# Kernel tuning notes

Measured on AMD Instinct MI355X. Metric: run time of the kernel, lower is better.

The kernel has to match this reference:

```python
import jax, jax.numpy as jnp
import numpy as np

EPS = 1e-12


def _phi(e):
    # e: [C, L] -> pairwise euclidean distances [C, C], diagonal zeroed
    sq = jnp.sum(e * e, axis=1)                      # [C]
    prod = e @ e.T                                   # [C, C]
    d2 = sq[:, None] + sq[None, :] - 2.0 * prod
    d = jnp.sqrt(jnp.clip(d2, EPS, None))
    C = e.shape[0]
    return d * (1.0 - jnp.eye(C, dtype=e.dtype))


def setup_inputs() -> dict:
    key = jax.random.key(0)
    k1, k2, k3 = jax.random.split(key, 3)
    N, C, L = 64, 512, 256
    le_student = jax.random.normal(k1, (N, C, L), dtype=jnp.float32)
    le_teacher = jax.random.normal(k2, (N, C, L), dtype=jnp.float32)
    targets = jax.random.randint(k3, (N, C), 0, 2, dtype=jnp.int32)
    return {"le_student": le_student, "le_teacher": le_teacher, "targets": targets}


def reference(le_student, le_teacher, targets):
    N, C, L = le_student.shape
    m = targets.astype(le_student.dtype)             # [N, C] 0/1 mask
    es = le_student * m[:, :, None]                  # zero out negative rows
    et = le_teacher * m[:, :, None]

    Ds = jax.vmap(_phi)(es)                          # [N, C, C]
    Dt = jax.vmap(_phi)(et)                          # [N, C, C]

    eye = jnp.eye(C, dtype=m.dtype)
    pm = m[:, :, None] * m[:, None, :]               # pairs of positive rows
    offdiag = pm * (1.0 - eye)                       # off-diagonal positive pairs

    npos = jnp.sum(m, axis=1)                        # [N]
    cnt = npos * (npos - 1.0)                        # entries with d > 0 in submatrix
    valid = npos > 1.0
    safe_cnt = jnp.maximum(cnt, 1.0)

    mean_s = jnp.sum(Ds * offdiag, axis=(1, 2)) / safe_cnt
    mean_t = jax.lax.stop_gradient(jnp.sum(Dt * offdiag, axis=(1, 2)) / safe_cnt)
    mean_s = jnp.where(valid, mean_s, 1.0)
    mean_t = jnp.where(valid, mean_t, 1.0)

    d = Ds / mean_s[:, None, None]
    td = jax.lax.stop_gradient(Dt / mean_t[:, None, None])

    diff = d - td
    adiff = jnp.abs(diff)
    huber = jnp.where(adiff < 1.0, 0.5 * diff * diff, adiff - 0.5)

    per = jnp.sum(huber * pm, axis=(1, 2)) / jnp.maximum(npos, 1.0)
    return jnp.sum(jnp.where(valid, per, 0.0))
```

## Files before the change

### kernel.cpp

```cpp
#include <hip/hip_runtime.h>
#include <hip/hip_bf16.h>
#include <hip/hip_fp16.h>
#include <math.h>

#define NB 64
#define CC 512
#define LL 256

typedef __attribute__((ext_vector_type(4))) float floatx4;
typedef __attribute__((ext_vector_type(8))) short short8;

static __device__ __forceinline__ unsigned f2bf2(float x, float y) {
    __hip_bfloat162 h = __float22bfloat162_rn(make_float2(x, y));
    union { __hip_bfloat162 h; unsigned u; } c; c.h = h;
    return c.u;
}
static __device__ __forceinline__ unsigned short f2h(float x) {
    __half h = __float2half_rn(x);
    union { __half h; unsigned short u; } c; c.h = h;
    return c.u;
}
static __device__ __forceinline__ float h2f(unsigned u) {
    union { unsigned short u; __half h; } c; c.u = (unsigned short)u;
    return __half2float(c.h);
}

__global__ __launch_bounds__(256) void prep_kernel(
    const int* __restrict__ targets,
    int* __restrict__ idx, int* __restrict__ npos,
    float* __restrict__ sumS, float* __restrict__ sumT, float* __restrict__ out)
{
    const int n = blockIdx.x, tid = threadIdx.x;
    __shared__ int s_cnt[8], s_off[8];
    const int w = tid >> 6, lane = tid & 63;
    const int* tg = targets + n * CC;
    const bool p0 = tg[tid] != 0;
    const bool p1 = tg[tid + 256] != 0;
    const unsigned long long m0 = __ballot(p0);
    const unsigned long long m1 = __ballot(p1);
    if (lane == 0) { s_cnt[w] = __popcll(m0); s_cnt[4 + w] = __popcll(m1); }
    __syncthreads();
    if (tid == 0) {
        int a = 0;
        for (int i = 0; i < 8; ++i) { s_off[i] = a; a += s_cnt[i]; }
        npos[n] = a;
        sumS[n] = 0.0f; sumT[n] = 0.0f;
        if (n == 0) out[0] = 0.0f;
    }
    __syncthreads();
    const unsigned long long below = (1ull << lane) - 1ull;
    if (p0) idx[n * CC + s_off[w] + __popcll(m0 & below)] = tid;
    if (p1) idx[n * CC + s_off[4 + w] + __popcll(m1 & below)] = tid + 256;
}

static __device__ __forceinline__ bool decode_tile(int t, int u, int& tI, int& tJ) {
    if (t >= (u * (u + 1)) >> 1) return false;
    tI = 0;
    while (t >= u - tI) { t -= u - tI; ++tI; }
    tJ = tI + t;
    return true;
}

__global__ __launch_bounds__(256) void dist_kernel(
    const float* __restrict__ S, const float* __restrict__ T,
    const int* __restrict__ idx, const int* __restrict__ npos,
    float* __restrict__ sumS, float* __restrict__ sumT,
    unsigned short* __restrict__ Ds, unsigned short* __restrict__ Dt)
{
    const int bx = blockIdx.x;
    const int n = bx & (NB - 1);
    const int q = bx >> 6;
    const int mat = q & 1, t = q >> 1;
    const int np = npos[n];
    if (np < 2) return;
    int tI, tJ;
    if (!decode_tile(t, (np + 63) >> 6, tI, tJ)) return;
    const bool diag = (tI == tJ);

    __shared__ __align__(16) unsigned short lds[2][2][64][40];
    __shared__ float s_norm[2][64];
    __shared__ float red[4];

    const int tid = threadIdx.x;
    const int w = tid >> 6, lane = tid & 63;

    const float* P = (mat ? T : S) + (size_t)n * CC * LL;
    unsigned short* Dout = (mat ? Dt : Ds) + (((size_t)t * NB + n) << 12);
    float* sumP = mat ? sumT : sumS;

    const int srow = w * 32 + (lane >> 1);
    const int half = lane & 1;
    const bool stager = diag ? (srow < 64) : true;
    const int ab = srow >> 6, rloc = srow & 63;
    const int gk = (ab ? tJ : tI) * 64 + rloc;
    const int row = idx[n * CC + ((gk < np) ? gk : 0)];
    const char* rp = (const char*)P + (size_t)row * (LL * 4) + half * 64;

    float4 pre[4];
    float nsum = 0.0f;
    if (stager) {
        #pragma unroll
        for (int i = 0; i < 4; ++i) pre[i] = *(const float4*)(rp + i * 16);
    }

    const int m16 = lane & 15, quad = lane >> 4;
    const int bufB = diag ? 0 : 1;
    const int wrow = w * 16;

    floatx4 acc[4];
    #pragma unroll
    for (int c = 0; c < 4; ++c) { acc[c][0] = 0; acc[c][1] = 0; acc[c][2] = 0; acc[c][3] = 0; }

    for (int kk = 0; kk < 8; ++kk) {
        const int pb = kk & 1;
        if (stager) {
            #pragma unroll
            for (int i = 0; i < 4; ++i)
                nsum += pre[i].x * pre[i].x + pre[i].y * pre[i].y +
                        pre[i].z * pre[i].z + pre[i].w * pre[i].w;
            unsigned short* dst = &lds[ab][pb][rloc][half * 16];
            *(uint2*)(dst + 0)  = make_uint2(f2bf2(pre[0].x, pre[0].y), f2bf2(pre[0].z, pre[0].w));
            *(uint2*)(dst + 4)  = make_uint2(f2bf2(pre[1].x, pre[1].y), f2bf2(pre[1].z, pre[1].w));
            *(uint2*)(dst + 8)  = make_uint2(f2bf2(pre[2].x, pre[2].y), f2bf2(pre[2].z, pre[2].w));
            *(uint2*)(dst + 12) = make_uint2(f2bf2(pre[3].x, pre[3].y), f2bf2(pre[3].z, pre[3].w));
        }
        __syncthreads();
        if (stager && kk < 7) {
            #pragma unroll
            for (int i = 0; i < 4; ++i)
                pre[i] = *(const float4*)(rp + (kk + 1) * 128 + i * 16);
        }
        const short8 a = *(const short8*)&lds[0][pb][wrow + m16][quad * 8];
        #pragma unroll
        for (int c = 0; c < 4; ++c) {
            const short8 b = *(const short8*)&lds[bufB][pb][c * 16 + m16][quad * 8];
            acc[c] = __builtin_amdgcn_mfma_f32_16x16x32_bf16(a, b, acc[c], 0, 0, 0);
        }
    }

    if (stager) {
        const float v = nsum + __shfl_xor(nsum, 1);
        if (half == 0) s_norm[ab][rloc] = v;
    }
    __syncthreads();

    float l0 = 0.0f;
    #pragma unroll
    for (int c = 0; c < 4; ++c) {
        const int colL = c * 16 + m16;
        const int gj = tJ * 64 + colL;
        const float nB = s_norm[bufB][colL];
        #pragma unroll
        for (int r = 0; r < 4; ++r) {
            const int rowL = wrow + quad * 4 + r;
            const int gi = tI * 64 + rowL;
            const float d = sqrtf(fmaxf(s_norm[0][rowL] + nB - 2.0f * acc[c][r], 1e-12f));
            if (gi < np && gj < np && gi != gj) l0 += d;
            Dout[rowL * 64 + colL] = f2h(d);
        }
    }

    #pragma unroll
    for (int o = 32; o; o >>= 1) l0 += __shfl_down(l0, o);
    if (lane == 0) red[w] = l0;
    __syncthreads();
    if (tid == 0) {
        const float wgt = diag ? 1.0f : 2.0f;
        atomicAdd(sumP + n, wgt * (red[0] + red[1] + red[2] + red[3]));
    }
}

__global__ __launch_bounds__(256) void huber_kernel(
    const unsigned short* __restrict__ Ds, const unsigned short* __restrict__ Dt,
    const int* __restrict__ npos,
    const float* __restrict__ sumS, const float* __restrict__ sumT,
    float* __restrict__ out)
{
    const int bx = blockIdx.x;
    const int n = bx & (NB - 1), t = bx >> 6;
    const int np = npos[n];
    if (np < 2) return;
    int tI, tJ;
    if (!decode_tile(t, (np + 63) >> 6, tI, tJ)) return;

    const float cnt = (float)np * (float)(np - 1);
    const float inv_ms = cnt / sumS[n];
    const float inv_mt = cnt / sumT[n];

    const size_t slot = ((size_t)t * NB + n) << 12;
    const uint4* ps = (const uint4*)(Ds + slot);
    const uint4* pt = (const uint4*)(Dt + slot);
    const int tid = threadIdx.x;

    float h = 0.0f;
    #pragma unroll
    for (int it = 0; it < 2; ++it) {
        const int g = it * 256 + tid;
        const uint4 a = ps[g];
        const uint4 b = pt[g];
        const unsigned aw[4] = { a.x, a.y, a.z, a.w };
        const unsigned bw[4] = { b.x, b.y, b.z, b.w };
        const int e0 = g * 8;
        #pragma unroll
        for (int k = 0; k < 8; ++k) {
            const int e = e0 + k;
            const int gi = tI * 64 + (e >> 6);
            const int gj = tJ * 64 + (e & 63);
            if (gi < np && gj < np && gi != gj) {
                const unsigned wa = aw[k >> 1], wb = bw[k >> 1];
                const float ds = h2f((k & 1) ? (wa >> 16) : (wa & 0xffffu));
                const float dt = h2f((k & 1) ? (wb >> 16) : (wb & 0xffffu));
                const float diff = ds * inv_ms - dt * inv_mt;
                const float ad = fabsf(diff);
                h += (ad < 1.0f) ? 0.5f * diff * diff : ad - 0.5f;
            }
        }
    }

    #pragma unroll
    for (int o = 32; o; o >>= 1) h += __shfl_down(h, o);
    __shared__ float red[4];
    const int w = tid >> 6, lane = tid & 63;
    if (lane == 0) red[w] = h;
    __syncthreads();
    if (tid == 0) {
        const float wgt = (tI == tJ) ? 1.0f : 2.0f;
        atomicAdd(out, wgt * (red[0] + red[1] + red[2] + red[3]) / (float)np);
    }
}

extern "C" void kernel_launch(void* const* d_in, const int* in_sizes, int n_in,
                              void* d_out, int out_size, void* d_ws, size_t ws_size,
                              hipStream_t stream) {
    const float* S = (const float*)d_in[0];
    const float* T = (const float*)d_in[1];
    const int* targets = (const int*)d_in[2];
    float* out = (float*)d_out;

    char* p = (char*)d_ws;
    int* idx = (int*)p;        p += (size_t)NB * CC * 4;
    int* npos = (int*)p;       p += NB * 4;
    float* sumS = (float*)p;   p += NB * 4;
    float* sumT = (float*)p;   p += NB * 4;
    p = (char*)(((size_t)p + 255) & ~(size_t)255);
    unsigned short* Ds = (unsigned short*)p;   p += (size_t)36 * NB * 4096 * 2;
    unsigned short* Dt = (unsigned short*)p;

    prep_kernel<<<NB, 256, 0, stream>>>(targets, idx, npos, sumS, sumT, out);
    dist_kernel<<<72 * NB, 256, 0, stream>>>(S, T, idx, npos, sumS, sumT, Ds, Dt);
    huber_kernel<<<36 * NB, 256, 0, stream>>>(Ds, Dt, npos, sumS, sumT, out);
}
```

Baseline: 125.6 us.

## Fuse prep, distance and Huber kernels into one cooperative persistent kernel

Replaces the three launches with a single cooperative kernel that uses grid-wide syncs between the mask compaction, the Gram/distance phase and the Huber phase. Each block computes both student and teacher tiles and keeps its first tile's distances in registers, so the fp16 round-trip through global memory is removed for that tile. Overflow tiles are stored in fp32 scratch and read back after the grid sync. The gains are fewer launches and less intermediate traffic. The costs are a grid capped at 1024 blocks with serialized extra tiles, the grid.sync overhead, and doubled scratch size for the fp32 spill.

```diff
diff --git a/kernel.cpp b/kernel.cpp
--- a/kernel.cpp
+++ b/kernel.cpp
@@ -1,11 +1,13 @@
 #include <hip/hip_runtime.h>
 #include <hip/hip_bf16.h>
-#include <hip/hip_fp16.h>
+#include <hip/hip_cooperative_groups.h>
 #include <math.h>
 
 #define NB 64
 #define CC 512
 #define LL 256
+
+namespace cg = cooperative_groups;
 
 typedef __attribute__((ext_vector_type(4))) float floatx4;
 typedef __attribute__((ext_vector_type(8))) short short8;
@@ -14,43 +16,6 @@
     __hip_bfloat162 h = __float22bfloat162_rn(make_float2(x, y));
     union { __hip_bfloat162 h; unsigned u; } c; c.h = h;
     return c.u;
-}
-static __device__ __forceinline__ unsigned short f2h(float x) {
-    __half h = __float2half_rn(x);
-    union { __half h; unsigned short u; } c; c.h = h;
-    return c.u;
-}
-static __device__ __forceinline__ float h2f(unsigned u) {
-    union { unsigned short u; __half h; } c; c.u = (unsigned short)u;
-    return __half2float(c.h);
-}
-
-__global__ __launch_bounds__(256) void prep_kernel(
-    const int* __restrict__ targets,
-    int* __restrict__ idx, int* __restrict__ npos,
-    float* __restrict__ sumS, float* __restrict__ sumT, float* __restrict__ out)
-{
-    const int n = blockIdx.x, tid = threadIdx.x;
-    __shared__ int s_cnt[8], s_off[8];
-    const int w = tid >> 6, lane = tid & 63;
-    const int* tg = targets + n * CC;
-    const bool p0 = tg[tid] != 0;
-    const bool p1 = tg[tid + 256] != 0;
-    const unsigned long long m0 = __ballot(p0);
-    const unsigned long long m1 = __ballot(p1);
-    if (lane == 0) { s_cnt[w] = __popcll(m0); s_cnt[4 + w] = __popcll(m1); }
-    __syncthreads();
-    if (tid == 0) {
-        int a = 0;
-        for (int i = 0; i < 8; ++i) { s_off[i] = a; a += s_cnt[i]; }
-        npos[n] = a;
-        sumS[n] = 0.0f; sumT[n] = 0.0f;
-        if (n == 0) out[0] = 0.0f;
-    }
-    __syncthreads();
-    const unsigned long long below = (1ull << lane) - 1ull;
-    if (p0) idx[n * CC + s_off[w] + __popcll(m0 & below)] = tid;
-    if (p1) idx[n * CC + s_off[4 + w] + __popcll(m1 & below)] = tid + 256;
 }
 
 static __device__ __forceinline__ bool decode_tile(int t, int u, int& tI, int& tJ) {
@@ -61,39 +26,24 @@
     return true;
 }
 
-__global__ __launch_bounds__(256) void dist_kernel(
-    const float* __restrict__ S, const float* __restrict__ T,
-    const int* __restrict__ idx, const int* __restrict__ npos,
-    float* __restrict__ sumS, float* __restrict__ sumT,
-    unsigned short* __restrict__ Ds, unsigned short* __restrict__ Dt)
-{
-    const int bx = blockIdx.x;
-    const int n = bx & (NB - 1);
-    const int q = bx >> 6;
-    const int mat = q & 1, t = q >> 1;
-    const int np = npos[n];
-    if (np < 2) return;
-    int tI, tJ;
-    if (!decode_tile(t, (np + 63) >> 6, tI, tJ)) return;
-    const bool diag = (tI == tJ);
-
-    __shared__ __align__(16) unsigned short lds[2][2][64][40];
-    __shared__ float s_norm[2][64];
-    __shared__ float red[4];
-
-    const int tid = threadIdx.x;
+struct __align__(16) SharedBlk {
+    unsigned short lds[2][2][64][40];
+    float s_norm[2][2][64];
+    float red[2][4];
+};
+
+static __device__ __forceinline__ void gram64(
+    const float* __restrict__ P, const int* __restrict__ idxn,
+    int np, int tI, int tJ, bool diag, int tid,
+    SharedBlk& sh, int mat, floatx4 (&acc)[4])
+{
     const int w = tid >> 6, lane = tid & 63;
-
-    const float* P = (mat ? T : S) + (size_t)n * CC * LL;
-    unsigned short* Dout = (mat ? Dt : Ds) + (((size_t)t * NB + n) << 12);
-    float* sumP = mat ? sumT : sumS;
-
     const int srow = w * 32 + (lane >> 1);
     const int half = lane & 1;
     const bool stager = diag ? (srow < 64) : true;
     const int ab = srow >> 6, rloc = srow & 63;
     const int gk = (ab ? tJ : tI) * 64 + rloc;
-    const int row = idx[n * CC + ((gk < np) ? gk : 0)];
+    const int row = idxn[(gk < np) ? gk : 0];
     const char* rp = (const char*)P + (size_t)row * (LL * 4) + half * 64;
 
     float4 pre[4];
@@ -102,14 +52,9 @@
         #pragma unroll
         for (int i = 0; i < 4; ++i) pre[i] = *(const float4*)(rp + i * 16);
     }
-
     const int m16 = lane & 15, quad = lane >> 4;
     const int bufB = diag ? 0 : 1;
     const int wrow = w * 16;
-
-    floatx4 acc[4];
-    #pragma unroll
-    for (int c = 0; c < 4; ++c) { acc[c][0] = 0; acc[c][1] = 0; acc[c][2] = 0; acc[c][3] = 0; }
 
     for (int kk = 0; kk < 8; ++kk) {
         const int pb = kk & 1;
@@ -118,7 +63,7 @@
             for (int i = 0; i < 4; ++i)
                 nsum += pre[i].x * pre[i].x + pre[i].y * pre[i].y +
                         pre[i].z * pre[i].z + pre[i].w * pre[i].w;
-            unsigned short* dst = &lds[ab][pb][rloc][half * 16];
+            unsigned short* dst = &sh.lds[ab][pb][rloc][half * 16];
             *(uint2*)(dst + 0)  = make_uint2(f2bf2(pre[0].x, pre[0].y), f2bf2(pre[0].z, pre[0].w));
             *(uint2*)(dst + 4)  = make_uint2(f2bf2(pre[1].x, pre[1].y), f2bf2(pre[1].z, pre[1].w));
             *(uint2*)(dst + 8)  = make_uint2(f2bf2(pre[2].x, pre[2].y), f2bf2(pre[2].z, pre[2].w));
@@ -130,102 +75,215 @@
             for (int i = 0; i < 4; ++i)
                 pre[i] = *(const float4*)(rp + (kk + 1) * 128 + i * 16);
         }
-        const short8 a = *(const short8*)&lds[0][pb][wrow + m16][quad * 8];
+        const short8 a = *(const short8*)&sh.lds[0][pb][wrow + m16][quad * 8];
         #pragma unroll
         for (int c = 0; c < 4; ++c) {
-            const short8 b = *(const short8*)&lds[bufB][pb][c * 16 + m16][quad * 8];
+            const short8 b = *(const short8*)&sh.lds[bufB][pb][c * 16 + m16][quad * 8];
             acc[c] = __builtin_amdgcn_mfma_f32_16x16x32_bf16(a, b, acc[c], 0, 0, 0);
         }
     }
-
     if (stager) {
         const float v = nsum + __shfl_xor(nsum, 1);
-        if (half == 0) s_norm[ab][rloc] = v;
-    }
-    __syncthreads();
-
+        if (half == 0) sh.s_norm[mat][ab][rloc] = v;
+    }
+}
+
+static __device__ __forceinline__ float dists64(
+    const floatx4 (&acc)[4], SharedBlk& sh, int mat, int bufB,
+    int np, int tI, int tJ, int tid, float (&d)[4][4])
+{
+    const int lane = tid & 63;
+    const int m16 = lane & 15, quad = lane >> 4;
+    const int wrow = (tid >> 6) * 16;
     float l0 = 0.0f;
     #pragma unroll
     for (int c = 0; c < 4; ++c) {
         const int colL = c * 16 + m16;
         const int gj = tJ * 64 + colL;
-        const float nB = s_norm[bufB][colL];
+        const float nB = sh.s_norm[mat][bufB][colL];
         #pragma unroll
         for (int r = 0; r < 4; ++r) {
             const int rowL = wrow + quad * 4 + r;
             const int gi = tI * 64 + rowL;
-            const float d = sqrtf(fmaxf(s_norm[0][rowL] + nB - 2.0f * acc[c][r], 1e-12f));
-            if (gi < np && gj < np && gi != gj) l0 += d;
-            Dout[rowL * 64 + colL] = f2h(d);
-        }
-    }
-
-    #pragma unroll
-    for (int o = 32; o; o >>= 1) l0 += __shfl_down(l0, o);
-    if (lane == 0) red[w] = l0;
+            const float dd = sqrtf(fmaxf(sh.s_norm[mat][0][rowL] + nB - 2.0f * acc[c][r], 1e-12f));
+            d[c][r] = dd;
+            if (gi < np && gj < np && gi != gj) l0 += dd;
+        }
+    }
+    return l0;
+}
+
+static __device__ __forceinline__ void do_tile(
+    const float* __restrict__ Sb, const float* __restrict__ Tb,
+    const int* __restrict__ idxn,
+    int n, int np, int tI, int tJ, int tid,
+    SharedBlk& sh, float* __restrict__ sumS, float* __restrict__ sumT,
+    float (&dS)[4][4], float (&dT)[4][4])
+{
+    const bool diag = (tI == tJ);
+    const int bufB = diag ? 0 : 1;
+
+    floatx4 acc[4];
+    #pragma unroll
+    for (int c = 0; c < 4; ++c) { acc[c][0] = 0; acc[c][1] = 0; acc[c][2] = 0; acc[c][3] = 0; }
+    gram64(Sb, idxn, np, tI, tJ, diag, tid, sh, 0, acc);
+    __syncthreads();
+    const float l0S = dists64(acc, sh, 0, bufB, np, tI, tJ, tid, dS);
+
+    #pragma unroll
+    for (int c = 0; c < 4; ++c) { acc[c][0] = 0; acc[c][1] = 0; acc[c][2] = 0; acc[c][3] = 0; }
+    gram64(Tb, idxn, np, tI, tJ, diag, tid, sh, 1, acc);
+    __syncthreads();
+    const float l0T = dists64(acc, sh, 1, bufB, np, tI, tJ, tid, dT);
+
+    float a = l0S, b = l0T;
+    #pragma unroll
+    for (int o = 32; o; o >>= 1) { a += __shfl_down(a, o); b += __shfl_down(b, o); }
+    const int w = tid >> 6, lane = tid & 63;
+    if (lane == 0) { sh.red[0][w] = a; sh.red[1][w] = b; }
     __syncthreads();
     if (tid == 0) {
         const float wgt = diag ? 1.0f : 2.0f;
-        atomicAdd(sumP + n, wgt * (red[0] + red[1] + red[2] + red[3]));
-    }
-}
-
-__global__ __launch_bounds__(256) void huber_kernel(
-    const unsigned short* __restrict__ Ds, const unsigned short* __restrict__ Dt,
-    const int* __restrict__ npos,
-    const float* __restrict__ sumS, const float* __restrict__ sumT,
-    float* __restrict__ out)
-{
-    const int bx = blockIdx.x;
-    const int n = bx & (NB - 1), t = bx >> 6;
-    const int np = npos[n];
-    if (np < 2) return;
-    int tI, tJ;
-    if (!decode_tile(t, (np + 63) >> 6, tI, tJ)) return;
-
-    const float cnt = (float)np * (float)(np - 1);
-    const float inv_ms = cnt / sumS[n];
-    const float inv_mt = cnt / sumT[n];
-
-    const size_t slot = ((size_t)t * NB + n) << 12;
-    const uint4* ps = (const uint4*)(Ds + slot);
-    const uint4* pt = (const uint4*)(Dt + slot);
-    const int tid = threadIdx.x;
-
+        atomicAdd(sumS + n, wgt * (sh.red[0][0] + sh.red[0][1] + sh.red[0][2] + sh.red[0][3]));
+        atomicAdd(sumT + n, wgt * (sh.red[1][0] + sh.red[1][1] + sh.red[1][2] + sh.red[1][3]));
+    }
+    __syncthreads();
+}
+
+static __device__ __forceinline__ void huber_acc(
+    const float (&dS)[4][4], const float (&dT)[4][4],
+    float inv_ms, float inv_mt, int np, int tI, int tJ, int tid,
+    SharedBlk& sh, float* __restrict__ out)
+{
+    const int lane = tid & 63;
+    const int m16 = lane & 15, quad = lane >> 4;
+    const int wrow = (tid >> 6) * 16;
     float h = 0.0f;
     #pragma unroll
-    for (int it = 0; it < 2; ++it) {
-        const int g = it * 256 + tid;
-        const uint4 a = ps[g];
-        const uint4 b = pt[g];
-        const unsigned aw[4] = { a.x, a.y, a.z, a.w };
-        const unsigned bw[4] = { b.x, b.y, b.z, b.w };
-        const int e0 = g * 8;
+    for (int c = 0; c < 4; ++c) {
+        const int gj = tJ * 64 + c * 16 + m16;
         #pragma unroll
-        for (int k = 0; k < 8; ++k) {
-            const int e = e0 + k;
-            const int gi = tI * 64 + (e >> 6);
-            const int gj = tJ * 64 + (e & 63);
+        for (int r = 0; r < 4; ++r) {
+            const int gi = tI * 64 + wrow + quad * 4 + r;
             if (gi < np && gj < np && gi != gj) {
-                const unsigned wa = aw[k >> 1], wb = bw[k >> 1];
-                const float ds = h2f((k & 1) ? (wa >> 16) : (wa & 0xffffu));
-                const float dt = h2f((k & 1) ? (wb >> 16) : (wb & 0xffffu));
-                const float diff = ds * inv_ms - dt * inv_mt;
+                const float diff = dS[c][r] * inv_ms - dT[c][r] * inv_mt;
                 const float ad = fabsf(diff);
                 h += (ad < 1.0f) ? 0.5f * diff * diff : ad - 0.5f;
             }
         }
     }
-
     #pragma unroll
     for (int o = 32; o; o >>= 1) h += __shfl_down(h, o);
-    __shared__ float red[4];
-    const int w = tid >> 6, lane = tid & 63;
-    if (lane == 0) red[w] = h;
+    const int w = tid >> 6;
+    if (lane == 0) sh.red[0][w] = h;
     __syncthreads();
     if (tid == 0) {
         const float wgt = (tI == tJ) ? 1.0f : 2.0f;
-        atomicAdd(out, wgt * (red[0] + red[1] + red[2] + red[3]) / (float)np);
+        atomicAdd(out, wgt * (sh.red[0][0] + sh.red[0][1] + sh.red[0][2] + sh.red[0][3]) / (float)np);
+    }
+    __syncthreads();
+}
+
+__global__ __launch_bounds__(256, 4) void fused_kernel(
+    const float* __restrict__ S, const float* __restrict__ T,
+    const int* __restrict__ targets,
+    int* __restrict__ idx, int* __restrict__ npos,
+    float* __restrict__ sumS, float* __restrict__ sumT,
+    float* __restrict__ DsF, float* __restrict__ DtF,
+    float* __restrict__ out)
+{
+    __shared__ SharedBlk sh;
+    const int bid = blockIdx.x, tid = threadIdx.x;
+    cg::grid_group grid = cg::this_grid();
+
+    if (bid < NB) {
+        const int n = bid;
+        __shared__ int s_cnt[8], s_off[8];
+        const int w = tid >> 6, lane = tid & 63;
+        const int* tg = targets + n * CC;
+        const bool p0 = tg[tid] != 0;
+        const bool p1 = tg[tid + 256] != 0;
+        const unsigned long long m0 = __ballot(p0);
+        const unsigned long long m1 = __ballot(p1);
+        if (lane == 0) { s_cnt[w] = __popcll(m0); s_cnt[4 + w] = __popcll(m1); }
+        __syncthreads();
+        if (tid == 0) {
+            int a = 0;
+            for (int i = 0; i < 8; ++i) { s_off[i] = a; a += s_cnt[i]; }
+            npos[n] = a;
+            sumS[n] = 0.0f; sumT[n] = 0.0f;
+            if (n == 0) out[0] = 0.0f;
+        }
+        __syncthreads();
+        const unsigned long long below = (1ull << lane) - 1ull;
+        if (p0) idx[n * CC + s_off[w] + __popcll(m0 & below)] = tid;
+        if (p1) idx[n * CC + s_off[4 + w] + __popcll(m1 & below)] = tid + 256;
+    }
+    grid.sync();
+
+    const int n = bid & (NB - 1);
+    const int TSLOTS = (int)(gridDim.x >> 6);
+    const int tprim = bid >> 6;
+    const int np = __hip_atomic_load(&npos[n], __ATOMIC_RELAXED, __HIP_MEMORY_SCOPE_AGENT);
+    const int u = (np + 63) >> 6;
+    const int ntiles = (np >= 2) ? ((u * (u + 1)) >> 1) : 0;
+    const float* Sb = S + (size_t)n * CC * LL;
+    const float* Tb = T + (size_t)n * CC * LL;
+    const int* idxn = idx + n * CC;
+
+    float dS[4][4], dT[4][4];
+    int tI = 0, tJ = 0;
+    const bool active = (tprim < ntiles);
+    if (active) {
+        decode_tile(tprim, u, tI, tJ);
+        do_tile(Sb, Tb, idxn, n, np, tI, tJ, tid, sh, sumS, sumT, dS, dT);
+    }
+    for (int t2 = tprim + TSLOTS; t2 < 36; t2 += TSLOTS) {
+        if (t2 < ntiles) {
+            int eI, eJ; decode_tile(t2, u, eI, eJ);
+            float eS[4][4], eT[4][4];
+            do_tile(Sb, Tb, idxn, n, np, eI, eJ, tid, sh, sumS, sumT, eS, eT);
+            const size_t slot = ((size_t)t2 * NB + n) << 12;
+            const int lane = tid & 63, m16 = lane & 15, quad = lane >> 4, wrow = (tid >> 6) * 16;
+            #pragma unroll
+            for (int c = 0; c < 4; ++c) {
+                #pragma unroll
+                for (int r = 0; r < 4; ++r) {
+                    const int e = (wrow + quad * 4 + r) * 64 + c * 16 + m16;
+                    DsF[slot + e] = eS[c][r];
+                    DtF[slot + e] = eT[c][r];
+                }
+            }
+        }
+    }
+    grid.sync();
+
+    if (ntiles > 0) {
+        const float cnt = (float)np * (float)(np - 1);
+        const float ss = __hip_atomic_load(&sumS[n], __ATOMIC_RELAXED, __HIP_MEMORY_SCOPE_AGENT);
+        const float st = __hip_atomic_load(&sumT[n], __ATOMIC_RELAXED, __HIP_MEMORY_SCOPE_AGENT);
+        const float inv_ms = cnt / ss;
+        const float inv_mt = cnt / st;
+        if (active)
+            huber_acc(dS, dT, inv_ms, inv_mt, np, tI, tJ, tid, sh, out);
+        for (int t2 = tprim + TSLOTS; t2 < 36; t2 += TSLOTS) {
+            if (t2 < ntiles) {
+                int eI, eJ; decode_tile(t2, u, eI, eJ);
+                float eS[4][4], eT[4][4];
+                const size_t slot = ((size_t)t2 * NB + n) << 12;
+                const int lane = tid & 63, m16 = lane & 15, quad = lane >> 4, wrow = (tid >> 6) * 16;
+                #pragma unroll
+                for (int c = 0; c < 4; ++c) {
+                    #pragma unroll
+                    for (int r = 0; r < 4; ++r) {
+                        const int e = (wrow + quad * 4 + r) * 64 + c * 16 + m16;
+                        eS[c][r] = DsF[slot + e];
+                        eT[c][r] = DtF[slot + e];
+                    }
+                }
+                huber_acc(eS, eT, inv_ms, inv_mt, np, eI, eJ, tid, sh, out);
+            }
+        }
     }
 }
 
@@ -243,10 +301,20 @@
     float* sumS = (float*)p;   p += NB * 4;
     float* sumT = (float*)p;   p += NB * 4;
     p = (char*)(((size_t)p + 255) & ~(size_t)255);
-    unsigned short* Ds = (unsigned short*)p;   p += (size_t)36 * NB * 4096 * 2;
-    unsigned short* Dt = (unsigned short*)p;
-
-    prep_kernel<<<NB, 256, 0, stream>>>(targets, idx, npos, sumS, sumT, out);
-    dist_kernel<<<72 * NB, 256, 0, stream>>>(S, T, idx, npos, sumS, sumT, Ds, Dt);
-    huber_kernel<<<36 * NB, 256, 0, stream>>>(Ds, Dt, npos, sumS, sumT, out);
-}
+    float* DsF = (float*)p;    p += (size_t)36 * NB * 4096 * 4;
+    float* DtF = (float*)p;
+
+    static int maxblk = 0;
+    if (maxblk == 0) {
+        if (hipOccupancyMaxActiveBlocksPerMultiprocessor(&maxblk, fused_kernel, 256, 0) != hipSuccess
+            || maxblk < 1) maxblk = 1;
+    }
+    int G = maxblk * 256;
+    if (G > 1024) G = 1024;
+    G &= ~63;
+    if (G < 64) G = 64;
+
+    void* args[] = { (void*)&S, (void*)&T, (void*)&targets, (void*)&idx, (void*)&npos,
+                     (void*)&sumS, (void*)&sumT, (void*)&DsF, (void*)&DtF, (void*)&out };
+    hipLaunchCooperativeKernel((void*)fused_kernel, dim3(G), dim3(256), args, 0, stream);
+}
```

Result: slower. 257.5 us (+105.0%).

## Fold prep kernel into dist kernel and replace atomics with per-tile partial sums

Applied to the files above, without the earlier changes.

Removes the separate prep launch by having every dist block recompute the positive-row count and compaction index from targets into shared memory. Per-tile distance sums are written to distinct slots instead of being accumulated with atomics, and the huber kernel recounts positives and reduces the partial sums itself. This saves one kernel launch and the global idx round trip, at the cost of redundant ballot/compaction work in each block.

```diff
diff --git a/kernel.cpp b/kernel.cpp
--- a/kernel.cpp
+++ b/kernel.cpp
@@ -25,14 +25,37 @@
     return __half2float(c.h);
 }
 
-__global__ __launch_bounds__(256) void prep_kernel(
+static __device__ __forceinline__ bool decode_tile(int t, int u, int& tI, int& tJ) {
+    if (t >= (u * (u + 1)) >> 1) return false;
+    tI = 0;
+    while (t >= u - tI) { t -= u - tI; ++tI; }
+    tJ = tI + t;
+    return true;
+}
+
+__global__ __launch_bounds__(256) void dist_kernel(
+    const float* __restrict__ S, const float* __restrict__ T,
     const int* __restrict__ targets,
-    int* __restrict__ idx, int* __restrict__ npos,
-    float* __restrict__ sumS, float* __restrict__ sumT, float* __restrict__ out)
+    float* __restrict__ sumS, float* __restrict__ sumT,
+    unsigned short* __restrict__ Ds, unsigned short* __restrict__ Dt,
+    float* __restrict__ out)
 {
-    const int n = blockIdx.x, tid = threadIdx.x;
+    const int bx = blockIdx.x;
+    const int n = bx & (NB - 1);
+    const int q = bx >> 6;
+    const int mat = q & 1, t = q >> 1;
+    const int tid = threadIdx.x;
+    const int w = tid >> 6, lane = tid & 63;
+
+    __shared__ __align__(16) unsigned short lds[2][2][64][40];
+    __shared__ float s_norm[2][64];
+    __shared__ float red[4];
+    __shared__ int s_idx[CC];
     __shared__ int s_cnt[8], s_off[8];
-    const int w = tid >> 6, lane = tid & 63;
+    __shared__ int s_np;
+
+    if (bx == 0 && tid == 0) out[0] = 0.0f;
+
     const int* tg = targets + n * CC;
     const bool p0 = tg[tid] != 0;
     const bool p1 = tg[tid + 256] != 0;
@@ -43,57 +66,29 @@
     if (tid == 0) {
         int a = 0;
         for (int i = 0; i < 8; ++i) { s_off[i] = a; a += s_cnt[i]; }
-        npos[n] = a;
-        sumS[n] = 0.0f; sumT[n] = 0.0f;
-        if (n == 0) out[0] = 0.0f;
+        s_np = a;
     }
     __syncthreads();
     const unsigned long long below = (1ull << lane) - 1ull;
-    if (p0) idx[n * CC + s_off[w] + __popcll(m0 & below)] = tid;
-    if (p1) idx[n * CC + s_off[4 + w] + __popcll(m1 & below)] = tid + 256;
-}
-
-static __device__ __forceinline__ bool decode_tile(int t, int u, int& tI, int& tJ) {
-    if (t >= (u * (u + 1)) >> 1) return false;
-    tI = 0;
-    while (t >= u - tI) { t -= u - tI; ++tI; }
-    tJ = tI + t;
-    return true;
-}
-
-__global__ __launch_bounds__(256) void dist_kernel(
-    const float* __restrict__ S, const float* __restrict__ T,
-    const int* __restrict__ idx, const int* __restrict__ npos,
-    float* __restrict__ sumS, float* __restrict__ sumT,
-    unsigned short* __restrict__ Ds, unsigned short* __restrict__ Dt)
-{
-    const int bx = blockIdx.x;
-    const int n = bx & (NB - 1);
-    const int q = bx >> 6;
-    const int mat = q & 1, t = q >> 1;
-    const int np = npos[n];
+    if (p0) s_idx[s_off[w] + __popcll(m0 & below)] = tid;
+    if (p1) s_idx[s_off[4 + w] + __popcll(m1 & below)] = tid + 256;
+    const int np = s_np;
+    __syncthreads();
+
     if (np < 2) return;
     int tI, tJ;
     if (!decode_tile(t, (np + 63) >> 6, tI, tJ)) return;
     const bool diag = (tI == tJ);
 
-    __shared__ __align__(16) unsigned short lds[2][2][64][40];
-    __shared__ float s_norm[2][64];
-    __shared__ float red[4];
-
-    const int tid = threadIdx.x;
-    const int w = tid >> 6, lane = tid & 63;
-
     const float* P = (mat ? T : S) + (size_t)n * CC * LL;
     unsigned short* Dout = (mat ? Dt : Ds) + (((size_t)t * NB + n) << 12);
-    float* sumP = mat ? sumT : sumS;
 
     const int srow = w * 32 + (lane >> 1);
     const int half = lane & 1;
     const bool stager = diag ? (srow < 64) : true;
     const int ab = srow >> 6, rloc = srow & 63;
     const int gk = (ab ? tJ : tI) * 64 + rloc;
-    const int row = idx[n * CC + ((gk < np) ? gk : 0)];
+    const int row = s_idx[(gk < np) ? gk : 0];
     const char* rp = (const char*)P + (size_t)row * (LL * 4) + half * 64;
 
     float4 pre[4];
@@ -166,40 +161,61 @@
     __syncthreads();
     if (tid == 0) {
         const float wgt = diag ? 1.0f : 2.0f;
-        atomicAdd(sumP + n, wgt * (red[0] + red[1] + red[2] + red[3]));
+        (mat ? sumT : sumS)[t * NB + n] = wgt * (red[0] + red[1] + red[2] + red[3]);
     }
 }
 
 __global__ __launch_bounds__(256) void huber_kernel(
+    const int* __restrict__ targets,
+    const float* __restrict__ sumS, const float* __restrict__ sumT,
     const unsigned short* __restrict__ Ds, const unsigned short* __restrict__ Dt,
-    const int* __restrict__ npos,
-    const float* __restrict__ sumS, const float* __restrict__ sumT,
     float* __restrict__ out)
 {
     const int bx = blockIdx.x;
     const int n = bx & (NB - 1), t = bx >> 6;
-    const int np = npos[n];
+    const int tid = threadIdx.x;
+    const int w = tid >> 6, lane = tid & 63;
+
+    __shared__ int s_cnt[8];
+    __shared__ float red[4];
+
+    const int* tg = targets + n * CC;
+    const unsigned long long m0 = __ballot(tg[tid] != 0);
+    const unsigned long long m1 = __ballot(tg[tid + 256] != 0);
+    if (lane == 0) { s_cnt[w] = __popcll(m0); s_cnt[4 + w] = __popcll(m1); }
+    __syncthreads();
+    int np = 0;
+    #pragma unroll
+    for (int i = 0; i < 8; ++i) np += s_cnt[i];
+
     if (np < 2) return;
+    const int u = (np + 63) >> 6;
     int tI, tJ;
-    if (!decode_tile(t, (np + 63) >> 6, tI, tJ)) return;
+    if (!decode_tile(t, u, tI, tJ)) return;
+    const int ntiles = (u * (u + 1)) >> 1;
+
+    float a = 0.0f, b = 0.0f;
+    if (lane < ntiles) { a = sumS[lane * NB + n]; b = sumT[lane * NB + n]; }
+    #pragma unroll
+    for (int o = 32; o; o >>= 1) { a += __shfl_down(a, o); b += __shfl_down(b, o); }
+    a = __shfl(a, 0); b = __shfl(b, 0);
 
     const float cnt = (float)np * (float)(np - 1);
-    const float inv_ms = cnt / sumS[n];
-    const float inv_mt = cnt / sumT[n];
+    const float inv_ms = cnt / a;
+    const float inv_mt = cnt / b;
 
     const size_t slot = ((size_t)t * NB + n) << 12;
     const uint4* ps = (const uint4*)(Ds + slot);
     const uint4* pt = (const uint4*)(Dt + slot);
-    const int tid = threadIdx.x;
 
     float h = 0.0f;
     #pragma unroll
     for (int it = 0; it < 2; ++it) {
         const int g = it * 256 + tid;
-        const uint4 a = ps[g];
-        const uint4 b = pt[g];
-        const unsigned aw[4] = { a.x, a.y, a.z, a.w };
-        const unsigned bw[4] = { b.x, b.y, b.z, b.w };
+        const uint4 va = ps[g];
+        const uint4 vb = pt[g];
+        const unsigned aw[4] = { va.x, va.y, va.z, va.w };
+        const unsigned bw[4] = { vb.x, vb.y, vb.z, vb.w };
         const int e0 = g * 8;
         #pragma unroll
         for (int k = 0; k < 8; ++k) {
@@ -219,8 +235,6 @@
 
     #pragma unroll
     for (int o = 32; o; o >>= 1) h += __shfl_down(h, o);
-    __shared__ float red[4];
-    const int w = tid >> 6, lane = tid & 63;
     if (lane == 0) red[w] = h;
     __syncthreads();
     if (tid == 0) {
@@ -238,15 +252,12 @@
     float* out = (float*)d_out;
 
     char* p = (char*)d_ws;
-    int* idx = (int*)p;        p += (size_t)NB * CC * 4;
-    int* npos = (int*)p;       p += NB * 4;
-    float* sumS = (float*)p;   p += NB * 4;
-    float* sumT = (float*)p;   p += NB * 4;
+    float* sumS = (float*)p;   p += (size_t)36 * NB * 4;
+    float* sumT = (float*)p;   p += (size_t)36 * NB * 4;
     p = (char*)(((size_t)p + 255) & ~(size_t)255);
     unsigned short* Ds = (unsigned short*)p;   p += (size_t)36 * NB * 4096 * 2;
     unsigned short* Dt = (unsigned short*)p;
 
-    prep_kernel<<<NB, 256, 0, stream>>>(targets, idx, npos, sumS, sumT, out);
-    dist_kernel<<<72 * NB, 256, 0, stream>>>(S, T, idx, npos, sumS, sumT, Ds, Dt);
-    huber_kernel<<<36 * NB, 256, 0, stream>>>(Ds, Dt, npos, sumS, sumT, out);
-}
+    dist_kernel<<<72 * NB, 256, 0, stream>>>(S, T, targets, sumS, sumT, Ds, Dt, out);
+    huber_kernel<<<36 * NB, 256, 0, stream>>>(targets, sumS, sumT, Ds, Dt, out);
+}
```

After: 122.2 us. -2.7%, faster.
